# Performance work log

Hardware: AMD Instinct MI355X
Metric: run time of the kernel (lower is better)

## Reference

```python
import jax, jax.numpy as jnp
import numpy as np

B = 4096      # batch size per view (init arg bs)
D = 256       # embedding dim
TEMP = 0.5    # init arg temp
EPS = 1e-8    # torch CosineSimilarity eps


def setup_inputs() -> dict:
    key = jax.random.key(0)
    k1, k2 = jax.random.split(key)
    return {
        "emb1": jax.random.normal(k1, (B, D), dtype=jnp.float32),
        "emb2": jax.random.normal(k2, (B, D), dtype=jnp.float32),
    }


def reference(emb1, emb2):
    # z: (2B, D)
    z = jnp.concatenate([emb1, emb2], axis=0)
    n = 2 * B
    # Cosine similarity as normalize + GEMM (same math as broadcast CosineSimilarity):
    # sim[i,j] = (z_i . z_j) / max(||z_i||*||z_j||, eps), then / temp
    norms = jnp.linalg.norm(z, axis=-1)                       # (2B,)
    denom = jnp.maximum(norms[:, None] * norms[None, :], EPS)  # (2B,2B)
    sim = (z @ z.T) / denom / TEMP                             # (2B,2B)

    idx = jnp.arange(n)
    # positives: diag(sim, +B) then diag(sim, -B) == sim[i, (i+B) mod 2B]
    pos = sim[idx, (idx + B) % n]                              # (2B,)

    # logits row i = [pos_i, negatives_i] = all sim[i,:] except the diagonal.
    # cross-entropy with label 0: loss_i = -pos_i + logsumexp(row without diag)
    diag_mask = idx[:, None] == idx[None, :]
    sim_masked = jnp.where(diag_mask, -jnp.inf, sim)
    lse = jax.nn.logsumexp(sim_masked, axis=-1)                # (2B,)

    loss = jnp.sum(lse - pos) / n   # CrossEntropyLoss(reduction='sum') / 2B
    return loss
```

## Files before the change

### kernel.cpp

```cpp
#include <hip/hip_runtime.h>
#include <hip/hip_bf16.h>


constexpr int kN  = 8192;
constexpr int kD  = 256;
constexpr int kBH = 4096;
constexpr int kChunks  = 32;
constexpr int kColsPer = kN / kChunks;
constexpr int kNT = kColsPer / 16;
constexpr float kSqrtScale = 1.6986436f;
constexpr float kLn2 = 0.6931471805599453f;

typedef __attribute__((ext_vector_type(8))) short bf16x8;
typedef __attribute__((ext_vector_type(4))) float f32x4;

__device__ __forceinline__ unsigned short f2bf(float f) {
  union { float f; unsigned u; } x;
  x.f = f;
  unsigned u = x.u;
  return (unsigned short)((u + 0x7FFFu + ((u >> 16) & 1u)) >> 16);
}
__device__ __forceinline__ float bf2f(unsigned short h) {
  union { unsigned u; float f; } x;
  x.u = ((unsigned)h) << 16;
  return x.f;
}
__device__ __forceinline__ void gload_lds16(const short* g, short* l) {
  __builtin_amdgcn_global_load_lds(
      (const __attribute__((address_space(1))) void*)g,
      (__attribute__((address_space(3))) void*)l, 16, 0, 0);
}

__global__ void k_normalize(const float* __restrict__ e1,
                            const float* __restrict__ e2,
                            unsigned short* __restrict__ zn,
                            float* __restrict__ s_sum) {
  if (blockIdx.x < 8) {
    float4 z4 = {0.f, 0.f, 0.f, 0.f};
    *reinterpret_cast<float4*>(s_sum + blockIdx.x * 1024 + threadIdx.x * 4) = z4;
  }
  const int wave = threadIdx.x >> 6;
  const int lane = threadIdx.x & 63;
  const int row  = blockIdx.x * 4 + wave;
  const float* src = (row < kBH) ? (e1 + (size_t)row * kD)
                                 : (e2 + (size_t)(row - kBH) * kD);
  float4 v = *reinterpret_cast<const float4*>(src + lane * 4);
  float ssq = v.x * v.x + v.y * v.y + v.z * v.z + v.w * v.w;
#pragma unroll
  for (int m = 1; m < 64; m <<= 1) ssq += __shfl_xor(ssq, m);
  const float invs = kSqrtScale / sqrtf(ssq);
  ushort4 o;
  o.x = f2bf(v.x * invs);
  o.y = f2bf(v.y * invs);
  o.z = f2bf(v.z * invs);
  o.w = f2bf(v.w * invs);
  const int g  = row >> 4;
  const int rr = row & 15;
  const size_t dst = (size_t)g * 4096 + (lane >> 3) * 512 +
                     ((lane >> 1) & 3) * 128 + rr * 8 + (lane & 1) * 4;
  *reinterpret_cast<ushort4*>(zn + dst) = o;
}

__global__ void k_pos(const unsigned short* __restrict__ zn,
                      float* __restrict__ pos_val,
                      float* __restrict__ dacc) {
  const int wave = threadIdx.x >> 6;
  const int lane = threadIdx.x & 63;
  const int i = blockIdx.x * 4 + wave;
  const int j = i + kBH;
  const int rr = i & 15;
  const size_t off = (size_t)(i >> 4) * 4096 + (lane >> 3) * 512 +
                     ((lane >> 1) & 3) * 128 + rr * 8 + (lane & 1) * 4;
  ushort4 ua = *reinterpret_cast<const ushort4*>(zn + off);
  ushort4 ub = *reinterpret_cast<const ushort4*>(zn + off + (size_t)256 * 4096);
  float dij = 0.f, dii = 0.f, djj = 0.f;
  const unsigned short* pa = &ua.x;
  const unsigned short* pb = &ub.x;
#pragma unroll
  for (int q = 0; q < 4; ++q) {
    const float a = bf2f(pa[q]);
    const float b = bf2f(pb[q]);
    dij += a * b;
    dii += a * a;
    djj += b * b;
  }
#pragma unroll
  for (int m = 1; m < 64; m <<= 1) {
    dij += __shfl_xor(dij, m);
    dii += __shfl_xor(dii, m);
    djj += __shfl_xor(djj, m);
  }
  if (lane == 0) {
    const float p = dij * kLn2;
    pos_val[i] = p;
    pos_val[j] = p;
    dacc[i] = dii;
    dacc[j] = djj;
  }
}

__global__ __launch_bounds__(256, 4)
void k_simlse(const unsigned short* __restrict__ zn,
              float* __restrict__ s_sum) {
  __shared__ __align__(16) short ldsB[4][4096];

  const int bid = blockIdx.x;
  const int rt  = bid >> 5;
  const int ch  = bid & 31;
  const int wave = threadIdx.x >> 6;
  const int lane = threadIdx.x & 63;
  const int l15 = lane & 15;
  const int lhi = lane >> 4;
  const int rowBase = rt * 128 + wave * 32;
  const int grpBase = ch * kNT;

  bf16x8 a0[8], a1[8];
  {
    const unsigned short* ap = zn + (size_t)(rowBase >> 4) * 4096 + lane * 8;
#pragma unroll
    for (int ks = 0; ks < 8; ++ks) {
      a0[ks] = *reinterpret_cast<const bf16x8*>(ap + ks * 512);
      a1[ks] = *reinterpret_cast<const bf16x8*>(ap + 4096 + ks * 512);
    }
  }

  auto stage = [&](int t) {
    const short* src = (const short*)zn +
                       (size_t)(grpBase + (t & (kNT - 1))) * 4096 + wave * 1024;
    short* dst = &ldsB[t & 3][wave * 1024];
    gload_lds16(src + lane * 8, dst);
    gload_lds16(src + 512 + lane * 8, dst + 512);
  };

  stage(0);
  stage(1);
  stage(2);
  asm volatile("s_waitcnt vmcnt(0)" ::: "memory");

  float sacc[2][4] = {{0.f,0.f,0.f,0.f},{0.f,0.f,0.f,0.f}};

#pragma unroll 1
  for (int t = 0; t < kNT; ++t) {
    __builtin_amdgcn_s_barrier();
    stage(t + 3);
    asm volatile("s_waitcnt vmcnt(6)" ::: "memory");
    __builtin_amdgcn_s_barrier();

    const short* bt = &ldsB[t & 3][0];
    bf16x8 b[8];
#pragma unroll
    for (int ks = 0; ks < 8; ++ks)
      b[ks] = *reinterpret_cast<const bf16x8*>(bt + ks * 512 + lane * 8);

    f32x4 acc0 = {0.f,0.f,0.f,0.f};
    f32x4 acc1 = {0.f,0.f,0.f,0.f};
#pragma unroll
    for (int ks = 0; ks < 8; ++ks) {
      acc0 = __builtin_amdgcn_mfma_f32_16x16x32_bf16(a0[ks], b[ks], acc0, 0, 0, 0);
      acc1 = __builtin_amdgcn_mfma_f32_16x16x32_bf16(a1[ks], b[ks], acc1, 0, 0, 0);
    }
#pragma unroll
    for (int j = 0; j < 4; ++j) {
      sacc[0][j] += exp2f(acc0[j]);
      sacc[1][j] += exp2f(acc1[j]);
    }
  }

#pragma unroll
  for (int s = 0; s < 2; ++s) {
#pragma unroll
    for (int j = 0; j < 4; ++j) {
      float sv = sacc[s][j];
#pragma unroll
      for (int m = 1; m < 16; m <<= 1) sv += __shfl_xor(sv, m);
      if (l15 == 0) {
        const int row = rowBase + s * 16 + lhi * 4 + j;
        atomicAdd(&s_sum[row], sv);
      }
    }
  }
}

__global__ void k_final(const float* __restrict__ s_sum,
                        const float* __restrict__ dacc,
                        const float* __restrict__ pos_val,
                        float* __restrict__ out) {
  __shared__ float red[16];
  float acc = 0.0f;
  for (int r = threadIdx.x; r < kN; r += 1024)
    acc += logf(s_sum[r] - exp2f(dacc[r])) - pos_val[r];
#pragma unroll
  for (int m = 1; m < 64; m <<= 1) acc += __shfl_xor(acc, m);
  const int wave = threadIdx.x >> 6;
  const int lane = threadIdx.x & 63;
  if (lane == 0) red[wave] = acc;
  __syncthreads();
  if (threadIdx.x == 0) {
    float t = 0.0f;
#pragma unroll
    for (int w = 0; w < 16; ++w) t += red[w];
    out[0] = t / (float)kN;
  }
}

extern "C" void kernel_launch(void* const* d_in, const int* in_sizes, int n_in,
                              void* d_out, int out_size, void* d_ws, size_t ws_size,
                              hipStream_t stream) {
  const float* e1 = (const float*)d_in[0];
  const float* e2 = (const float*)d_in[1];
  float* out = (float*)d_out;

  unsigned short* zn = (unsigned short*)d_ws;
  float* s_sum   = (float*)((char*)d_ws + (size_t)kN * kD * 2);
  float* dacc    = s_sum + kN;
  float* pos_val = dacc + kN;

  hipLaunchKernelGGL(k_normalize, dim3(kN / 4), dim3(256), 0, stream,
                     e1, e2, zn, s_sum);
  hipLaunchKernelGGL(k_pos, dim3(kBH / 4), dim3(256), 0, stream,
                     zn, pos_val, dacc);
  hipLaunchKernelGGL(k_simlse, dim3(64 * kChunks), dim3(256), 0, stream,
                     zn, s_sum);
  hipLaunchKernelGGL(k_final, dim3(1), dim3(1024), 0, stream,
                     s_sum, dacc, pos_val, out);
}
```

Baseline: 57.80 us.

## Use 2-wave blocks with 64 rows per wave to double B-tile reuse

Shrinks the sim/LSE block from 4 to 2 waves, each holding 64 rows of A (4 row groups) in registers, so every B fragment read from LDS feeds four MFMAs instead of two. All 128 threads now cooperatively stage B tiles, which means four async copies per thread and a matching vmcnt. MFMA sections are wrapped in s_setprio, and A is loaded through inline asm. The change doubles A-register use per wave (64 VGPRs for A plus four accumulators), which lowers occupancy. It also leaves fewer waves to hide LDS and global latency.

```diff
diff --git a/kernel.cpp b/kernel.cpp
--- a/kernel.cpp
+++ b/kernel.cpp
@@ -29,6 +29,12 @@
   __builtin_amdgcn_global_load_lds(
       (const __attribute__((address_space(1))) void*)g,
       (__attribute__((address_space(3))) void*)l, 16, 0, 0);
+}
+__device__ __forceinline__ bf16x8 gload16(const unsigned short* p) {
+  bf16x8 r;
+  asm volatile("global_load_dwordx4 %0, %1, off"
+               : "=v"(r) : "v"(p) : "memory");
+  return r;
 }
 
 __global__ void k_normalize(const float* __restrict__ e1,
@@ -99,7 +105,7 @@
   }
 }
 
-__global__ __launch_bounds__(256, 4)
+__global__ __launch_bounds__(128, 2)
 void k_simlse(const unsigned short* __restrict__ zn,
               float* __restrict__ s_sum) {
   __shared__ __align__(16) short ldsB[4][4096];
@@ -107,29 +113,31 @@
   const int bid = blockIdx.x;
   const int rt  = bid >> 5;
   const int ch  = bid & 31;
-  const int wave = threadIdx.x >> 6;
-  const int lane = threadIdx.x & 63;
+  const int tid = threadIdx.x;
+  const int wave = tid >> 6;
+  const int lane = tid & 63;
   const int l15 = lane & 15;
   const int lhi = lane >> 4;
-  const int rowBase = rt * 128 + wave * 32;
+  const int rowBase = rt * 128 + wave * 64;
   const int grpBase = ch * kNT;
 
-  bf16x8 a0[8], a1[8];
+  bf16x8 a[4][8];
   {
     const unsigned short* ap = zn + (size_t)(rowBase >> 4) * 4096 + lane * 8;
 #pragma unroll
-    for (int ks = 0; ks < 8; ++ks) {
-      a0[ks] = *reinterpret_cast<const bf16x8*>(ap + ks * 512);
-      a1[ks] = *reinterpret_cast<const bf16x8*>(ap + 4096 + ks * 512);
-    }
+    for (int g = 0; g < 4; ++g)
+#pragma unroll
+      for (int ks = 0; ks < 8; ++ks)
+        a[g][ks] = gload16(ap + g * 4096 + ks * 512);
   }
 
   auto stage = [&](int t) {
     const short* src = (const short*)zn +
-                       (size_t)(grpBase + (t & (kNT - 1))) * 4096 + wave * 1024;
-    short* dst = &ldsB[t & 3][wave * 1024];
-    gload_lds16(src + lane * 8, dst);
-    gload_lds16(src + 512 + lane * 8, dst + 512);
+                       (size_t)(grpBase + (t & (kNT - 1))) * 4096;
+    short* dst = &ldsB[t & 3][0];
+#pragma unroll
+    for (int r = 0; r < 4; ++r)
+      gload_lds16(src + r * 1024 + tid * 8, dst + r * 1024 + tid * 8);
   };
 
   stage(0);
@@ -137,13 +145,17 @@
   stage(2);
   asm volatile("s_waitcnt vmcnt(0)" ::: "memory");
 
-  float sacc[2][4] = {{0.f,0.f,0.f,0.f},{0.f,0.f,0.f,0.f}};
+  float sacc[4][4];
+#pragma unroll
+  for (int g = 0; g < 4; ++g)
+#pragma unroll
+    for (int j = 0; j < 4; ++j) sacc[g][j] = 0.f;
 
 #pragma unroll 1
   for (int t = 0; t < kNT; ++t) {
     __builtin_amdgcn_s_barrier();
     stage(t + 3);
-    asm volatile("s_waitcnt vmcnt(6)" ::: "memory");
+    asm volatile("s_waitcnt vmcnt(12)" ::: "memory");
     __builtin_amdgcn_s_barrier();
 
     const short* bt = &ldsB[t & 3][0];
@@ -152,29 +164,35 @@
     for (int ks = 0; ks < 8; ++ks)
       b[ks] = *reinterpret_cast<const bf16x8*>(bt + ks * 512 + lane * 8);
 
-    f32x4 acc0 = {0.f,0.f,0.f,0.f};
-    f32x4 acc1 = {0.f,0.f,0.f,0.f};
+    f32x4 acc[4];
+#pragma unroll
+    for (int g = 0; g < 4; ++g) acc[g] = {0.f, 0.f, 0.f, 0.f};
+    __builtin_amdgcn_s_setprio(1);
 #pragma unroll
     for (int ks = 0; ks < 8; ++ks) {
-      acc0 = __builtin_amdgcn_mfma_f32_16x16x32_bf16(a0[ks], b[ks], acc0, 0, 0, 0);
-      acc1 = __builtin_amdgcn_mfma_f32_16x16x32_bf16(a1[ks], b[ks], acc1, 0, 0, 0);
+      const bf16x8 bk = b[ks];
+#pragma unroll
+      for (int g = 0; g < 4; ++g)
+        acc[g] = __builtin_amdgcn_mfma_f32_16x16x32_bf16(a[g][ks], bk, acc[g], 0, 0, 0);
     }
+    __builtin_amdgcn_s_setprio(0);
+
+#pragma unroll
+    for (int g = 0; g < 4; ++g)
+#pragma unroll
+      for (int j = 0; j < 4; ++j)
+        sacc[g][j] += exp2f(acc[g][j]);
+  }
+
+#pragma unroll
+  for (int g = 0; g < 4; ++g) {
 #pragma unroll
     for (int j = 0; j < 4; ++j) {
-      sacc[0][j] += exp2f(acc0[j]);
-      sacc[1][j] += exp2f(acc1[j]);
-    }
-  }
-
-#pragma unroll
-  for (int s = 0; s < 2; ++s) {
-#pragma unroll
-    for (int j = 0; j < 4; ++j) {
-      float sv = sacc[s][j];
+      float sv = sacc[g][j];
 #pragma unroll
       for (int m = 1; m < 16; m <<= 1) sv += __shfl_xor(sv, m);
       if (l15 == 0) {
-        const int row = rowBase + s * 16 + lhi * 4 + j;
+        const int row = rowBase + g * 16 + lhi * 4 + j;
         atomicAdd(&s_sum[row], sv);
       }
     }
@@ -219,7 +237,7 @@
                      e1, e2, zn, s_sum);
   hipLaunchKernelGGL(k_pos, dim3(kBH / 4), dim3(256), 0, stream,
                      zn, pos_val, dacc);
-  hipLaunchKernelGGL(k_simlse, dim3(64 * kChunks), dim3(256), 0, stream,
+  hipLaunchKernelGGL(k_simlse, dim3(64 * kChunks), dim3(128), 0, stream,
                      zn, s_sum);
   hipLaunchKernelGGL(k_final, dim3(1), dim3(1024), 0, stream,
                      s_sum, dacc, pos_val, out);
```

Result: slower. 66.29 us (+14.7%).
